# Kernel tuning notes

Measured on AMD Instinct MI355X. Metric: run time of the kernel, lower is better.

Reference implementation:

```python
import jax, jax.numpy as jnp
import numpy as np
import math

L, B, T, S, D, H = 6, 4, 1024, 1024, 1024, 16
HD = D // H
SCALE = 1.0 / math.sqrt(HD)
EPS = 1e-5


def _ln(x, w, b):
    m = x.mean(-1, keepdims=True)
    v = ((x - m) ** 2).mean(-1, keepdims=True)
    return (x - m) * jax.lax.rsqrt(v + EPS) * w + b


def _mha(xq, xkv, qw, qb, kw, kb, vw, vb, ow, ob, mask):
    b, t, _ = xq.shape
    s = xkv.shape[1]
    q = (xq @ qw.T + qb).reshape(b, t, H, HD).transpose(0, 2, 1, 3)
    k = (xkv @ kw.T + kb).reshape(b, s, H, HD).transpose(0, 2, 1, 3)
    v = (xkv @ vw.T + vb).reshape(b, s, H, HD).transpose(0, 2, 1, 3)
    scores = jnp.einsum('bhqd,bhkd->bhqk', q, k) * SCALE
    scores = jnp.where(mask == 0, -jnp.inf, scores)
    attn = jax.nn.softmax(scores, axis=-1)  # dropout is identity (eval)
    o = jnp.einsum('bhqk,bhkd->bhqd', attn, v).transpose(0, 2, 1, 3).reshape(b, t, D)
    return o @ ow.T + ob


def _ffn(x, f1w, f1b, f2w, f2b, fnw, fnb):
    h = jax.nn.gelu(x @ f1w.T + f1b, approximate=False)
    y = h @ f2w.T + f2b
    return x + _ln(y, fnw, fnb)


def setup_inputs() -> dict:
    key = jax.random.key(0)
    ks = jax.random.split(key, 16)
    wf = lambda k: jax.random.normal(k, (L, D, D), jnp.float32) * 0.02
    zb = jnp.zeros((L, D), jnp.float32)
    ones = jnp.ones((L, D), jnp.float32)
    inp = {
        'x': jax.random.normal(ks[0], (B, T, D), jnp.float32),
        'enc_outputs': jax.random.normal(ks[1], (B, S, D), jnp.float32),
        'sqw': wf(ks[2]), 'sqb': zb, 'skw': wf(ks[3]), 'skb': zb,
        'svw': wf(ks[4]), 'svb': zb, 'sow': wf(ks[5]), 'sob': zb,
        'cqw': wf(ks[6]), 'cqb': zb, 'ckw': wf(ks[7]), 'ckb': zb,
        'cvw': wf(ks[8]), 'cvb': zb, 'cow': wf(ks[9]), 'cob': zb,
        'f1w': wf(ks[10]), 'f1b': zb, 'f2w': wf(ks[11]), 'f2b': zb,
        'fnw': ones, 'fnb': zb,
        'l1w': ones, 'l1b': zb, 'l2w': ones, 'l2b': zb, 'l3w': ones, 'l3b': zb,
        'src_mask': jnp.ones((1, 1, T, S), jnp.int32),
        'tgt_mask': jnp.tril(jnp.ones((T, T), jnp.int32))[None, None],
    }
    return inp


def reference(x, enc_outputs, sqw, sqb, skw, skb, svw, svb, sow, sob,
              cqw, cqb, ckw, ckb, cvw, cvb, cow, cob,
              f1w, f1b, f2w, f2b, fnw, fnb,
              l1w, l1b, l2w, l2b, l3w, l3b, src_mask, tgt_mask):
    for l in range(L):
        sa = _mha(x, x, sqw[l], sqb[l], skw[l], skb[l], svw[l], svb[l], sow[l], sob[l], tgt_mask)
        x = _ln(x + sa, l1w[l], l1b[l])
        ca = _mha(x, enc_outputs, cqw[l], cqb[l], ckw[l], ckb[l], cvw[l], cvb[l], cow[l], cob[l], src_mask)
        x = _ln(x + ca, l2w[l], l2b[l])
        ff = _ffn(x, f1w[l], f1b[l], f2w[l], f2b[l], fnw[l], fnb[l])
        x = _ln(x + ff, l3w[l], l3b[l])
    return x
```

## Files before the change

kernel.cpp:

```cpp
#include <hip/hip_runtime.h>
#include <stdint.h>

typedef unsigned short u16;
typedef unsigned int u32;
typedef __bf16 bf16x8 __attribute__((ext_vector_type(8)));
typedef float f32x4 __attribute__((ext_vector_type(4)));
typedef u16 u16x8 __attribute__((ext_vector_type(8)));
typedef u16 u16x4 __attribute__((ext_vector_type(4)));
typedef u32 u32x2 __attribute__((ext_vector_type(2)));

#define MFMA16(A, B, C) __builtin_amdgcn_mfma_f32_16x16x32_bf16((A), (B), (C), 0, 0, 0)

#define GLOAD_LDS16(GP, LP)                                                    \
  __builtin_amdgcn_global_load_lds(                                            \
      (__attribute__((address_space(1))) void*)(GP),                           \
      (__attribute__((address_space(3))) void*)(LP), 16, 0, 0)

__device__ __forceinline__ u16 f2bf(float f) {
  return __builtin_bit_cast(u16, (__bf16)f);
}

__device__ __forceinline__ float bf2f(u16 v) {
  return __builtin_bit_cast(float, ((u32)v) << 16);
}

__device__ __forceinline__ float exp2_raw(float x) {
  float r;
  asm("v_exp_f32 %0, %1\n\ts_nop 0" : "=v"(r) : "v"(x));
  return r;
}

__device__ __forceinline__ u32 cvt_pk_bf16(float lo, float hi) {
  u32 r;
  asm("v_cvt_pk_bf16_f32 %0, %1, %2" : "=v"(r) : "v"(lo), "v"(hi));
  return r;
}

#define SC2 0.1803368801111204f

struct WPtrs {
  const float* p[10];
};

__global__ __launch_bounds__(256) void wcvt_kernel(WPtrs w, u16* __restrict__ dst, int loff) {
  const int mat = blockIdx.y;
  const int i = blockIdx.x * 256 + threadIdx.x;
  float4 v = ((const float4*)(w.p[mat] + loff))[i];
  u16x4 o = {f2bf(v.x), f2bf(v.y), f2bf(v.z), f2bf(v.w)};
  ((u16x4*)dst)[(size_t)mat * gridDim.x * 256 + i] = o;
}

struct GemmArgs {
  const u16* A[3];
  const u16* W[3];
  const float* bias[3];
  u16* C[3];
  float scale[3];
};

__global__ __launch_bounds__(256, 4) void gemm_bt(GemmArgs g) {
  const int mat = blockIdx.y >> 3;
  const int n0 = (blockIdx.y & 7) * 128;
  const int m0 = blockIdx.x * 128;
  const int kz = blockIdx.z;
  const int kn = 16 / gridDim.z;
  const u16* __restrict__ A = g.A[mat];
  const u16* __restrict__ W = g.W[mat];

  __shared__ u16 As[128][64];
  __shared__ u16 Bs[128][64];

  const int tid = threadIdx.x;
  const int lane = tid & 63;
  const int wv = tid >> 6;
  const int wm = (wv >> 1) * 64;
  const int wn = (wv & 1) * 64;
  const int fr = lane & 15;
  const int fg = lane >> 4;

  f32x4 acc[4][4];
#pragma unroll
  for (int i = 0; i < 4; ++i)
#pragma unroll
    for (int j = 0; j < 4; ++j)
#pragma unroll
      for (int r = 0; r < 4; ++r) acc[i][j][r] = 0.f;

  const int row8 = lane >> 3;
  const int csw = ((lane & 7) ^ row8) * 8;
  const u16* ga = A + (size_t)(m0 + wv * 32 + row8) * 1024 + csw + kz * kn * 64;
  const u16* gb = W + (size_t)(n0 + wv * 32 + row8) * 1024 + csw + kz * kn * 64;

  for (int kt = 0; kt < kn; ++kt) {
    __syncthreads();
#pragma unroll
    for (int i = 0; i < 4; ++i) {
      GLOAD_LDS16(ga + (size_t)i * 8 * 1024, &As[wv * 32 + i * 8][0]);
      GLOAD_LDS16(gb + (size_t)i * 8 * 1024, &Bs[wv * 32 + i * 8][0]);
    }
    ga += 64;
    gb += 64;
    __syncthreads();
#pragma unroll
    for (int ks = 0; ks < 2; ++ks) {
      bf16x8 af[4], bfr[4];
#pragma unroll
      for (int i = 0; i < 4; ++i) {
        af[i] = *(const bf16x8*)&As[wm + i * 16 + fr][((ks * 4 + fg) ^ (fr & 7)) * 8];
        bfr[i] = *(const bf16x8*)&Bs[wn + i * 16 + fr][((ks * 4 + fg) ^ (fr & 7)) * 8];
      }
#pragma unroll
      for (int mi = 0; mi < 4; ++mi)
#pragma unroll
        for (int ni = 0; ni < 4; ++ni) acc[mi][ni] = MFMA16(af[mi], bfr[ni], acc[mi][ni]);
    }
  }

  const float* __restrict__ bias = g.bias[mat];
  const float scl = g.scale[mat];
  float bv[4];
#pragma unroll
  for (int ni = 0; ni < 4; ++ni) bv[ni] = (kz == 0) ? bias[n0 + wn + ni * 16 + fr] : 0.f;

  u16* __restrict__ C = g.C[mat] + (size_t)kz * (4096 * 1024);
#pragma unroll
  for (int mi = 0; mi < 4; ++mi) {
#pragma unroll
    for (int ni = 0; ni < 4; ++ni) {
      const int col = n0 + wn + ni * 16 + fr;
#pragma unroll
      for (int r = 0; r < 4; ++r) {
        const int row = m0 + wm + mi * 16 + fg * 4 + r;
        C[(size_t)row * 1024 + col] = f2bf((acc[mi][ni][r] + bv[ni]) * scl);
      }
    }
  }
}

__global__ __launch_bounds__(256, 4) void gemm_ckv(const u16* __restrict__ A,
                                                   const u16* __restrict__ wbf,
                                                   const float* __restrict__ ckb,
                                                   const float* __restrict__ cvb,
                                                   u16* __restrict__ ckv) {
  const int m = blockIdx.y >> 3;
  const int l = m >> 1;
  const int ty = m & 1;
  const int n0 = (blockIdx.y & 7) * 128;
  const int m0 = blockIdx.x * 128;
  const u16* __restrict__ W = wbf + ((size_t)(5 + ty) * 6 + l) * (1024 * 1024);
  const float* __restrict__ bias = (ty ? cvb : ckb) + l * 1024;
  u16* __restrict__ C = ckv + (size_t)m * (4096 * 1024);

  __shared__ u16 As[128][64];
  __shared__ u16 Bs[128][64];

  const int tid = threadIdx.x;
  const int lane = tid & 63;
  const int wv = tid >> 6;
  const int wm = (wv >> 1) * 64;
  const int wn = (wv & 1) * 64;
  const int fr = lane & 15;
  const int fg = lane >> 4;

  f32x4 acc[4][4];
#pragma unroll
  for (int i = 0; i < 4; ++i)
#pragma unroll
    for (int j = 0; j < 4; ++j)
#pragma unroll
      for (int r = 0; r < 4; ++r) acc[i][j][r] = 0.f;

  const int row8 = lane >> 3;
  const int csw = ((lane & 7) ^ row8) * 8;
  const u16* ga = A + (size_t)(m0 + wv * 32 + row8) * 1024 + csw;
  const u16* gb = W + (size_t)(n0 + wv * 32 + row8) * 1024 + csw;

  for (int kt = 0; kt < 16; ++kt) {
    __syncthreads();
#pragma unroll
    for (int i = 0; i < 4; ++i) {
      GLOAD_LDS16(ga + (size_t)i * 8 * 1024, &As[wv * 32 + i * 8][0]);
      GLOAD_LDS16(gb + (size_t)i * 8 * 1024, &Bs[wv * 32 + i * 8][0]);
    }
    ga += 64;
    gb += 64;
    __syncthreads();
#pragma unroll
    for (int ks = 0; ks < 2; ++ks) {
      bf16x8 af[4], bfr[4];
#pragma unroll
      for (int i = 0; i < 4; ++i) {
        af[i] = *(const bf16x8*)&As[wm + i * 16 + fr][((ks * 4 + fg) ^ (fr & 7)) * 8];
        bfr[i] = *(const bf16x8*)&Bs[wn + i * 16 + fr][((ks * 4 + fg) ^ (fr & 7)) * 8];
      }
#pragma unroll
      for (int mi = 0; mi < 4; ++mi)
#pragma unroll
        for (int ni = 0; ni < 4; ++ni) acc[mi][ni] = MFMA16(af[mi], bfr[ni], acc[mi][ni]);
    }
  }

  float bv[4];
#pragma unroll
  for (int ni = 0; ni < 4; ++ni) bv[ni] = bias[n0 + wn + ni * 16 + fr];
#pragma unroll
  for (int mi = 0; mi < 4; ++mi) {
#pragma unroll
    for (int ni = 0; ni < 4; ++ni) {
      const int col = n0 + wn + ni * 16 + fr;
#pragma unroll
      for (int r = 0; r < 4; ++r) {
        const int row = m0 + wm + mi * 16 + fg * 4 + r;
        C[(size_t)row * 1024 + col] = f2bf(acc[mi][ni][r] + bv[ni]);
      }
    }
  }
}

__global__ __launch_bounds__(512, 4) void attn_fwd(const u16* __restrict__ Q,
                                                   const u16* __restrict__ K,
                                                   const u16* __restrict__ V,
                                                   u16* __restrict__ O, int causal) {
  const int b = blockIdx.x >> 4;
  const int h = blockIdx.x & 15;
  const int qb = causal ? (7 - blockIdx.y) : blockIdx.y;
  const int tid = threadIdx.x;
  const int lane = tid & 63;
  const int wv = tid >> 6;
  const int fr = lane & 15;
  const int fg = lane >> 4;

  __shared__ u16 Ks[2][64][64];
  __shared__ u16 Vt[2][64][64];
  __shared__ u16 Plds[8][16][64];

  const int qrow0 = b * 1024 + qb * 128 + wv * 16;
  const int col0 = h * 64;

  const u16* qp = Q + (size_t)(qrow0 + fr) * 1024 + col0 + fg * 8;
  bf16x8 aQ0 = *(const bf16x8*)qp;
  bf16x8 aQ1 = *(const bf16x8*)(qp + 32);

  f32x4 ov[4];
#pragma unroll
  for (int i = 0; i < 4; ++i)
#pragma unroll
    for (int r = 0; r < 4; ++r) ov[i][r] = 0.f;
  float l_part = 0.f;

  const int kv_base = b * 1024;
  const int qg = qb * 128 + wv * 16 + fr;
  const int qg_max = qb * 128 + wv * 16 + 15;
  const int nt = causal ? (2 * qb + 2) : 16;

  const u16* gk0 = K + (size_t)(kv_base + wv * 16 + (lane >> 3)) * 1024 + col0 +
                   (((lane & 7) ^ (lane >> 3)) * 8);
  const int vt = tid - 256;
  const int kkp = vt & 31;
  const int d0 = (vt >> 5) * 8;
  const u16* gv0 = V + (size_t)(kv_base + 2 * kkp) * 1024 + col0 + d0;

#define STAGE_K(T, BUF)                                                        \
  if (wv < 4) {                                                                \
    const u16* gk = gk0 + (size_t)(T)*64 * 1024;                               \
    GLOAD_LDS16(gk, &Ks[BUF][wv * 16][0]);                                     \
    GLOAD_LDS16(gk + 8 * 1024, &Ks[BUF][wv * 16 + 8][0]);                      \
  }
#define LOAD_V(T)                                                              \
  if (tid >= 256) {                                                            \
    const u16* gvp = gv0 + (size_t)(T)*64 * 1024;                              \
    vr0 = *(const u16x8*)gvp;                                                  \
    vr1 = *(const u16x8*)(gvp + 1024);                                         \
  }
#define WRITE_V(BUF)                                                           \
  if (tid >= 256) {                                                            \
    _Pragma("unroll") for (int j = 0; j < 8; ++j) {                            \
      u32 pk = (u32)vr0[j] | ((u32)vr1[j] << 16);                              \
      *(u32*)&Vt[BUF][d0 + j][(((kkp >> 2) ^ j) * 8) + (kkp & 3) * 2] = pk;    \
    }                                                                          \
  }

  u16x8 vr0, vr1;
  STAGE_K(0, 0);
  LOAD_V(0);
  WRITE_V(0);

  for (int t = 0; t < nt; ++t) {
    const int cur = t & 1;
    __syncthreads();
    const bool pf = (t + 1 < nt);
    if (pf) {
      STAGE_K(t + 1, cur ^ 1);
      LOAD_V(t + 1);
    }

    const bool active = !causal || (t * 64 <= qg_max);
    if (active) {
      f32x4 st[4];
      __builtin_amdgcn_s_setprio(1);
#pragma unroll
      for (int hh = 0; hh < 4; ++hh) {
#pragma unroll
        for (int r = 0; r < 4; ++r) st[hh][r] = 0.f;
        const u16* krow = &Ks[cur][hh * 16 + fr][0];
        bf16x8 k0 = *(const bf16x8*)(krow + ((fg ^ (fr & 7)) * 8));
        bf16x8 k1 = *(const bf16x8*)(krow + (((4 + fg) ^ (fr & 7)) * 8));
        st[hh] = MFMA16(k0, aQ0, st[hh]);
        st[hh] = MFMA16(k1, aQ1, st[hh]);
      }
      __builtin_amdgcn_s_setprio(0);

      if (causal && t >= 2 * qb) {
#pragma unroll
        for (int hh = 0; hh < 4; ++hh)
#pragma unroll
          for (int r = 0; r < 4; ++r) {
            const int kkg = t * 64 + hh * 16 + fg * 4 + r;
            if (kkg > qg) st[hh][r] = -1e30f;
          }
      }

      float p[16];
#pragma unroll
      for (int hh = 0; hh < 4; ++hh)
#pragma unroll
        for (int r = 0; r < 4; ++r) {
          const float e = exp2_raw(st[hh][r]);
          p[hh * 4 + r] = e;
          l_part += e;
        }

#pragma unroll
      for (int hh = 0; hh < 4; ++hh) {
        u32x2 wpair = {cvt_pk_bf16(p[hh * 4 + 0], p[hh * 4 + 1]),
                       cvt_pk_bf16(p[hh * 4 + 2], p[hh * 4 + 3])};
        const int c = hh * 2 + (fg >> 1);
        *(u32x2*)&Plds[wv][fr][((c ^ (fr & 7)) * 8) + (fg & 1) * 4] = wpair;
      }
      bf16x8 pa[2];
#pragma unroll
      for (int ks = 0; ks < 2; ++ks)
        pa[ks] = *(const bf16x8*)&Plds[wv][fr][(((ks * 4 + fg) ^ (fr & 7)) * 8)];
      __builtin_amdgcn_s_setprio(1);
#pragma unroll
      for (int dt = 0; dt < 4; ++dt) {
#pragma unroll
        for (int ks = 0; ks < 2; ++ks) {
          bf16x8 bvv =
              *(const bf16x8*)&Vt[cur][dt * 16 + fr][(((ks * 4 + fg) ^ (fr & 7)) * 8)];
          ov[dt] = MFMA16(pa[ks], bvv, ov[dt]);
        }
      }
      __builtin_amdgcn_s_setprio(0);
    }

    if (pf) WRITE_V(cur ^ 1);
  }

  float ps = l_part;
  ps += __shfl_xor(ps, 16);
  ps += __shfl_xor(ps, 32);
  const float linv = 1.0f / ps;
  float fin[4];
#pragma unroll
  for (int r = 0; r < 4; ++r) fin[r] = __shfl(linv, fg * 4 + r);
#pragma unroll
  for (int dt = 0; dt < 4; ++dt)
#pragma unroll
    for (int r = 0; r < 4; ++r) {
      const int row = qrow0 + fg * 4 + r;
      const int col = col0 + dt * 16 + fr;
      O[(size_t)row * 1024 + col] = f2bf(ov[dt][r] * fin[r]);
    }
#undef STAGE_K
#undef LOAD_V
#undef WRITE_V
}

__device__ __forceinline__ float4 ld_bf4(const u16* p, size_t idx4) {
  u16x4 t = ((const u16x4*)p)[idx4];
  return make_float4(bf2f(t[0]), bf2f(t[1]), bf2f(t[2]), bf2f(t[3]));
}

__global__ __launch_bounds__(256) void ln_res_kernel(const u16* __restrict__ Xb_in,
                                                     const u16* __restrict__ T0,
                                                     const u16* __restrict__ T1, int nT,
                                                     const float* __restrict__ w,
                                                     const float* __restrict__ bia,
                                                     u16* __restrict__ Xb_out) {
  __shared__ float red[2][4];
  const int row = blockIdx.x;
  const int tid = threadIdx.x;
  const int lane = tid & 63, wv = tid >> 6;
  const size_t base4 = (size_t)row * 256;
  float4 xv = ld_bf4(Xb_in, base4 + tid);
  float4 tv = ld_bf4(T0, base4 + tid);
  float z0 = xv.x + tv.x, z1 = xv.y + tv.y, z2 = xv.z + tv.z, z3 = xv.w + tv.w;
  if (nT == 2) {
    float4 t1 = ld_bf4(T1, base4 + tid);
    z0 += t1.x; z1 += t1.y; z2 += t1.z; z3 += t1.w;
  }
  float s = z0 + z1 + z2 + z3;
  float ss = z0 * z0 + z1 * z1 + z2 * z2 + z3 * z3;
#pragma unroll
  for (int m = 1; m <= 32; m <<= 1) {
    s += __shfl_xor(s, m);
    ss += __shfl_xor(ss, m);
  }
  if (lane == 0) {
    red[0][wv] = s;
    red[1][wv] = ss;
  }
  __syncthreads();
  s = red[0][0] + red[0][1] + red[0][2] + red[0][3];
  ss = red[1][0] + red[1][1] + red[1][2] + red[1][3];
  const float mean = s * (1.f / 1024.f);
  const float var = ss * (1.f / 1024.f) - mean * mean;
  const float rs = rsqrtf(fmaxf(var, 0.f) + 1e-5f);
  float4 wv4 = ((const float4*)w)[tid];
  float4 bv4 = ((const float4*)bia)[tid];
  float o0 = (z0 - mean) * rs * wv4.x + bv4.x;
  float o1 = (z1 - mean) * rs * wv4.y + bv4.y;
  float o2 = (z2 - mean) * rs * wv4.z + bv4.z;
  float o3 = (z3 - mean) * rs * wv4.w + bv4.w;
  u16x4 ob = {f2bf(o0), f2bf(o1), f2bf(o2), f2bf(o3)};
  ((u16x4*)Xb_out)[base4 + tid] = ob;
}

__global__ __launch_bounds__(256) void ffn_ln_kernel(
    const u16* __restrict__ Xb, const u16* __restrict__ Y0, const u16* __restrict__ Y1,
    int nT, const float* __restrict__ fw_, const float* __restrict__ fb_,
    const float* __restrict__ w3, const float* __restrict__ b3, u16* __restrict__ Xb_out,
    float* __restrict__ Fout) {
  __shared__ float red[2][4];
  const int row = blockIdx.x;
  const int tid = threadIdx.x;
  const int lane = tid & 63, wv = tid >> 6;
  const size_t base4 = (size_t)row * 256;
  float4 yv = ld_bf4(Y0, base4 + tid);
  if (nT == 2) {
    float4 y1 = ld_bf4(Y1, base4 + tid);
    yv.x += y1.x; yv.y += y1.y; yv.z += y1.z; yv.w += y1.w;
  }
  float s = yv.x + yv.y + yv.z + yv.w;
  float ss = yv.x * yv.x + yv.y * yv.y + yv.z * yv.z + yv.w * yv.w;
#pragma unroll
  for (int m = 1; m <= 32; m <<= 1) {
    s += __shfl_xor(s, m);
    ss += __shfl_xor(ss, m);
  }
  if (lane == 0) {
    red[0][wv] = s;
    red[1][wv] = ss;
  }
  __syncthreads();
  s = red[0][0] + red[0][1] + red[0][2] + red[0][3];
  ss = red[1][0] + red[1][1] + red[1][2] + red[1][3];
  const float mean = s * (1.f / 1024.f);
  const float var = ss * (1.f / 1024.f) - mean * mean;
  const float rs = rsqrtf(fmaxf(var, 0.f) + 1e-5f);
  float4 xv = ld_bf4(Xb, base4 + tid);
  float4 fw4 = ((const float4*)fw_)[tid];
  float4 fb4 = ((const float4*)fb_)[tid];
  float z0 = 2.f * xv.x + (yv.x - mean) * rs * fw4.x + fb4.x;
  float z1 = 2.f * xv.y + (yv.y - mean) * rs * fw4.y + fb4.y;
  float z2 = 2.f * xv.z + (yv.z - mean) * rs * fw4.z + fb4.z;
  float z3 = 2.f * xv.w + (yv.w - mean) * rs * fw4.w + fb4.w;
  float s2 = z0 + z1 + z2 + z3;
  float ss2 = z0 * z0 + z1 * z1 + z2 * z2 + z3 * z3;
#pragma unroll
  for (int m = 1; m <= 32; m <<= 1) {
    s2 += __shfl_xor(s2, m);
    ss2 += __shfl_xor(ss2, m);
  }
  __syncthreads();
  if (lane == 0) {
    red[0][wv] = s2;
    red[1][wv] = ss2;
  }
  __syncthreads();
  s2 = red[0][0] + red[0][1] + red[0][2] + red[0][3];
  ss2 = red[1][0] + red[1][1] + red[1][2] + red[1][3];
  const float mean2 = s2 * (1.f / 1024.f);
  const float var2 = ss2 * (1.f / 1024.f) - mean2 * mean2;
  const float rs2 = rsqrtf(fmaxf(var2, 0.f) + 1e-5f);
  float4 w4 = ((const float4*)w3)[tid];
  float4 b4 = ((const float4*)b3)[tid];
  float o0 = (z0 - mean2) * rs2 * w4.x + b4.x;
  float o1 = (z1 - mean2) * rs2 * w4.y + b4.y;
  float o2 = (z2 - mean2) * rs2 * w4.z + b4.z;
  float o3 = (z3 - mean2) * rs2 * w4.w + b4.w;
  u16x4 ob = {f2bf(o0), f2bf(o1), f2bf(o2), f2bf(o3)};
  ((u16x4*)Xb_out)[base4 + tid] = ob;
  if (Fout) ((float4*)Fout)[base4 + tid] = make_float4(o0, o1, o2, o3);
}

__global__ __launch_bounds__(256) void gelu_combine(const u16* __restrict__ T0,
                                                    const u16* __restrict__ T1, int nT,
                                                    u16* __restrict__ dst) {
  const size_t i = (size_t)blockIdx.x * 256 + threadIdx.x;
  float4 v = ld_bf4(T0, i);
  if (nT == 2) {
    float4 u = ld_bf4(T1, i);
    v.x += u.x; v.y += u.y; v.z += u.z; v.w += u.w;
  }
  v.x = 0.5f * v.x * (1.0f + erff(v.x * 0.70710678118654752f));
  v.y = 0.5f * v.y * (1.0f + erff(v.y * 0.70710678118654752f));
  v.z = 0.5f * v.z * (1.0f + erff(v.z * 0.70710678118654752f));
  v.w = 0.5f * v.w * (1.0f + erff(v.w * 0.70710678118654752f));
  u16x4 o = {f2bf(v.x), f2bf(v.y), f2bf(v.z), f2bf(v.w)};
  ((u16x4*)dst)[i] = o;
}

__global__ __launch_bounds__(256) void cast2_kernel(const float* __restrict__ inA,
                                                    const float* __restrict__ inB,
                                                    u16* __restrict__ outA,
                                                    u16* __restrict__ outB) {
  const int bx = blockIdx.x;
  const float* in = (bx < 4096) ? inA : inB;
  u16* out = (bx < 4096) ? outA : outB;
  const size_t i = (size_t)(bx & 4095) * 256 + threadIdx.x;
  float4 v = ((const float4*)in)[i];
  u16x4 o = {f2bf(v.x), f2bf(v.y), f2bf(v.z), f2bf(v.w)};
  ((u16x4*)out)[i] = o;
}

extern "C" void kernel_launch(void* const* d_in, const int* in_sizes, int n_in, void* d_out,
                              int out_size, void* d_ws, size_t ws_size, hipStream_t stream) {
  const float* x_in = (const float*)d_in[0];
  const float* enc = (const float*)d_in[1];
  const float* sqw = (const float*)d_in[2];
  const float* sqb = (const float*)d_in[3];
  const float* skw = (const float*)d_in[4];
  const float* skb = (const float*)d_in[5];
  const float* svw = (const float*)d_in[6];
  const float* svb = (const float*)d_in[7];
  const float* sow = (const float*)d_in[8];
  const float* sob = (const float*)d_in[9];
  const float* cqw = (const float*)d_in[10];
  const float* cqb = (const float*)d_in[11];
  const float* ckw = (const float*)d_in[12];
  const float* ckb = (const float*)d_in[13];
  const float* cvw = (const float*)d_in[14];
  const float* cvb = (const float*)d_in[15];
  const float* cow = (const float*)d_in[16];
  const float* cob = (const float*)d_in[17];
  const float* f1w = (const float*)d_in[18];
  const float* f1b = (const float*)d_in[19];
  const float* f2w = (const float*)d_in[20];
  const float* f2b = (const float*)d_in[21];
  const float* fnw = (const float*)d_in[22];
  const float* fnb = (const float*)d_in[23];
  const float* l1w = (const float*)d_in[24];
  const float* l1b = (const float*)d_in[25];
  const float* l2w = (const float*)d_in[26];
  const float* l2b = (const float*)d_in[27];
  const float* l3w = (const float*)d_in[28];
  const float* l3b = (const float*)d_in[29];

  const size_t MB = 1024 * 1024;
  const int ALLW = (ws_size >= 200 * MB) ? 1 : 0;
  const int NS = (ws_size >= 90 * MB) ? 2 : 1;
  const int CKV = (ALLW && ws_size >= 273 * MB) ? 1 : 0;
  char* ws = (char*)d_ws;
  u16* tmpb = (u16*)ws;
  char* p = ws + (size_t)NS * 8 * MB;
  u16* xb = (u16*)p;   p += 8 * MB;
  u16* encb = (u16*)p; p += 8 * MB;
  u16* qbuf = (u16*)p; p += 8 * MB;
  u16* kbuf = (u16*)p; p += 8 * MB;
  u16* vbuf = (u16*)p; p += 8 * MB;
  u16* wbf = (u16*)p;  p += (ALLW ? 120 : 20) * MB;
  u16* ckv = (u16*)p;
  u16* tmpb1 = tmpb + (size_t)4 * 1024 * 1024;
  const size_t W1M = 1024 * 1024;

  cast2_kernel<<<8192, 256, 0, stream>>>(x_in, enc, xb, encb);

  WPtrs wp;
  wp.p[0] = sqw; wp.p[1] = skw; wp.p[2] = svw; wp.p[3] = sow;
  wp.p[4] = cqw; wp.p[5] = ckw; wp.p[6] = cvw; wp.p[7] = cow;
  wp.p[8] = f1w; wp.p[9] = f2w;

  if (ALLW) wcvt_kernel<<<dim3(6144, 10), 256, 0, stream>>>(wp, wbf, 0);
  if (CKV) gemm_ckv<<<dim3(32, 96), 256, 0, stream>>>(encb, wbf, ckb, cvb, ckv);

  for (int l = 0; l < 6; ++l) {
    const size_t bo = (size_t)l * 1024;
    if (!ALLW) wcvt_kernel<<<dim3(1024, 10), 256, 0, stream>>>(wp, wbf, l * (int)W1M);
    #define WT(t) (ALLW ? (wbf + ((size_t)(t)*6 + l) * W1M) : (wbf + (size_t)(t)*W1M))

    GemmArgs g;
    g.scale[0] = SC2; g.scale[1] = 1.f; g.scale[2] = 1.f;
    g.A[0] = xb; g.A[1] = xb; g.A[2] = xb;
    g.W[0] = WT(0); g.W[1] = WT(1); g.W[2] = WT(2);
    g.bias[0] = sqb + bo; g.bias[1] = skb + bo; g.bias[2] = svb + bo;
    g.C[0] = qbuf; g.C[1] = kbuf; g.C[2] = vbuf;
    gemm_bt<<<dim3(32, 24, 1), 256, 0, stream>>>(g);
    attn_fwd<<<dim3(64, 8), 512, 0, stream>>>(qbuf, kbuf, vbuf, qbuf, 1);
    g.scale[0] = 1.f;
    g.A[0] = qbuf; g.W[0] = WT(3); g.bias[0] = sob + bo; g.C[0] = tmpb;
    gemm_bt<<<dim3(32, 8, NS), 256, 0, stream>>>(g);
    ln_res_kernel<<<4096, 256, 0, stream>>>(xb, tmpb, tmpb1, NS, l1w + bo, l1b + bo, xb);

    g.scale[0] = SC2;
    const u16 *ck_l, *cv_l;
    if (CKV) {
      g.A[0] = xb;
      g.W[0] = WT(4);
      g.bias[0] = cqb + bo;
      g.C[0] = qbuf;
      gemm_bt<<<dim3(32, 8, 1), 256, 0, stream>>>(g);
      ck_l = ckv + (size_t)(2 * l) * (4096 * 1024);
      cv_l = ckv + (size_t)(2 * l + 1) * (4096 * 1024);
    } else {
      g.A[0] = xb; g.A[1] = encb; g.A[2] = encb;
      g.W[0] = WT(4); g.W[1] = WT(5); g.W[2] = WT(6);
      g.bias[0] = cqb + bo; g.bias[1] = ckb + bo; g.bias[2] = cvb + bo;
      g.C[0] = qbuf; g.C[1] = kbuf; g.C[2] = vbuf;
      gemm_bt<<<dim3(32, 24, 1), 256, 0, stream>>>(g);
      ck_l = kbuf;
      cv_l = vbuf;
    }
    attn_fwd<<<dim3(64, 8), 512, 0, stream>>>(qbuf, ck_l, cv_l, qbuf, 0);
    g.scale[0] = 1.f;
    g.A[0] = qbuf; g.W[0] = WT(7); g.bias[0] = cob + bo; g.C[0] = tmpb;
    gemm_bt<<<dim3(32, 8, NS), 256, 0, stream>>>(g);
    ln_res_kernel<<<4096, 256, 0, stream>>>(xb, tmpb, tmpb1, NS, l2w + bo, l2b + bo, xb);

    g.A[0] = xb; g.W[0] = WT(8); g.bias[0] = f1b + bo; g.C[0] = tmpb;
    gemm_bt<<<dim3(32, 8, NS), 256, 0, stream>>>(g);
    gelu_combine<<<4096, 256, 0, stream>>>(tmpb, tmpb1, NS, kbuf);
    g.A[0] = kbuf; g.W[0] = WT(9); g.bias[0] = f2b + bo; g.C[0] = tmpb;
    gemm_bt<<<dim3(32, 8, NS), 256, 0, stream>>>(g);
    float* fo = (l == 5) ? (float*)d_out : nullptr;
    ffn_ln_kernel<<<4096, 256, 0, stream>>>(xb, tmpb, tmpb1, NS, fnw + bo, fnb + bo, l3w + bo,
                                            l3b + bo, xb, fo);
    #undef WT
  }
}
```

Measured before the change: 1.478 ms.

## Use 64x128 tiles for single-matrix GEMMs and drop precomputed cross-attention K/V

Adds a gemm_bt64 kernel with 64-row M tiles (2x4 MFMA per wave) and uses it for the output projections and both FFN GEMMs, doubling the block count to 512-1024 to fill more CUs. It also removes the upfront all-layer cross-attention K/V precompute (gemm_ckv and its workspace), so each layer computes cross Q/K/V in one fused launch again. Smaller tiles lower per-block operand reuse and add more A/B traffic. Dropping the precompute moves K/V work back into the layer loop.

```diff
diff --git a/kernel.cpp b/kernel.cpp
--- a/kernel.cpp
+++ b/kernel.cpp
@@ -137,34 +137,28 @@
   }
 }
 
-__global__ __launch_bounds__(256, 4) void gemm_ckv(const u16* __restrict__ A,
-                                                   const u16* __restrict__ wbf,
-                                                   const float* __restrict__ ckb,
-                                                   const float* __restrict__ cvb,
-                                                   u16* __restrict__ ckv) {
-  const int m = blockIdx.y >> 3;
-  const int l = m >> 1;
-  const int ty = m & 1;
-  const int n0 = (blockIdx.y & 7) * 128;
-  const int m0 = blockIdx.x * 128;
-  const u16* __restrict__ W = wbf + ((size_t)(5 + ty) * 6 + l) * (1024 * 1024);
-  const float* __restrict__ bias = (ty ? cvb : ckb) + l * 1024;
-  u16* __restrict__ C = ckv + (size_t)m * (4096 * 1024);
-
-  __shared__ u16 As[128][64];
+__global__ __launch_bounds__(256, 4) void gemm_bt64(GemmArgs g) {
+  const int n0 = blockIdx.y * 128;
+  const int m0 = blockIdx.x * 64;
+  const int kz = blockIdx.z;
+  const int kn = 16 / gridDim.z;
+  const u16* __restrict__ A = g.A[0];
+  const u16* __restrict__ W = g.W[0];
+
+  __shared__ u16 As[64][64];
   __shared__ u16 Bs[128][64];
 
   const int tid = threadIdx.x;
   const int lane = tid & 63;
   const int wv = tid >> 6;
-  const int wm = (wv >> 1) * 64;
+  const int wm = (wv >> 1) * 32;
   const int wn = (wv & 1) * 64;
   const int fr = lane & 15;
   const int fg = lane >> 4;
 
-  f32x4 acc[4][4];
-#pragma unroll
-  for (int i = 0; i < 4; ++i)
+  f32x4 acc[2][4];
+#pragma unroll
+  for (int i = 0; i < 2; ++i)
 #pragma unroll
     for (int j = 0; j < 4; ++j)
 #pragma unroll
@@ -172,39 +166,43 @@
 
   const int row8 = lane >> 3;
   const int csw = ((lane & 7) ^ row8) * 8;
-  const u16* ga = A + (size_t)(m0 + wv * 32 + row8) * 1024 + csw;
-  const u16* gb = W + (size_t)(n0 + wv * 32 + row8) * 1024 + csw;
-
-  for (int kt = 0; kt < 16; ++kt) {
+  const u16* ga = A + (size_t)(m0 + wv * 16 + row8) * 1024 + csw + kz * kn * 64;
+  const u16* gb = W + (size_t)(n0 + wv * 32 + row8) * 1024 + csw + kz * kn * 64;
+
+  for (int kt = 0; kt < kn; ++kt) {
     __syncthreads();
-#pragma unroll
-    for (int i = 0; i < 4; ++i) {
-      GLOAD_LDS16(ga + (size_t)i * 8 * 1024, &As[wv * 32 + i * 8][0]);
+    GLOAD_LDS16(ga, &As[wv * 16][0]);
+    GLOAD_LDS16(ga + (size_t)8 * 1024, &As[wv * 16 + 8][0]);
+#pragma unroll
+    for (int i = 0; i < 4; ++i)
       GLOAD_LDS16(gb + (size_t)i * 8 * 1024, &Bs[wv * 32 + i * 8][0]);
-    }
     ga += 64;
     gb += 64;
     __syncthreads();
 #pragma unroll
     for (int ks = 0; ks < 2; ++ks) {
-      bf16x8 af[4], bfr[4];
-#pragma unroll
-      for (int i = 0; i < 4; ++i) {
+      bf16x8 af[2], bfr[4];
+#pragma unroll
+      for (int i = 0; i < 2; ++i)
         af[i] = *(const bf16x8*)&As[wm + i * 16 + fr][((ks * 4 + fg) ^ (fr & 7)) * 8];
+#pragma unroll
+      for (int i = 0; i < 4; ++i)
         bfr[i] = *(const bf16x8*)&Bs[wn + i * 16 + fr][((ks * 4 + fg) ^ (fr & 7)) * 8];
-      }
-#pragma unroll
-      for (int mi = 0; mi < 4; ++mi)
+#pragma unroll
+      for (int mi = 0; mi < 2; ++mi)
 #pragma unroll
         for (int ni = 0; ni < 4; ++ni) acc[mi][ni] = MFMA16(af[mi], bfr[ni], acc[mi][ni]);
     }
   }
 
+  const float* __restrict__ bias = g.bias[0];
   float bv[4];
 #pragma unroll
-  for (int ni = 0; ni < 4; ++ni) bv[ni] = bias[n0 + wn + ni * 16 + fr];
-#pragma unroll
-  for (int mi = 0; mi < 4; ++mi) {
+  for (int ni = 0; ni < 4; ++ni) bv[ni] = (kz == 0) ? bias[n0 + wn + ni * 16 + fr] : 0.f;
+
+  u16* __restrict__ C = g.C[0] + (size_t)kz * (4096 * 1024);
+#pragma unroll
+  for (int mi = 0; mi < 2; ++mi) {
 #pragma unroll
     for (int ni = 0; ni < 4; ++ni) {
       const int col = n0 + wn + ni * 16 + fr;
@@ -561,7 +559,6 @@
   const size_t MB = 1024 * 1024;
   const int ALLW = (ws_size >= 200 * MB) ? 1 : 0;
   const int NS = (ws_size >= 90 * MB) ? 2 : 1;
-  const int CKV = (ALLW && ws_size >= 273 * MB) ? 1 : 0;
   char* ws = (char*)d_ws;
   u16* tmpb = (u16*)ws;
   char* p = ws + (size_t)NS * 8 * MB;
@@ -570,8 +567,7 @@
   u16* qbuf = (u16*)p; p += 8 * MB;
   u16* kbuf = (u16*)p; p += 8 * MB;
   u16* vbuf = (u16*)p; p += 8 * MB;
-  u16* wbf = (u16*)p;  p += (ALLW ? 120 : 20) * MB;
-  u16* ckv = (u16*)p;
+  u16* wbf = (u16*)p;
   u16* tmpb1 = tmpb + (size_t)4 * 1024 * 1024;
   const size_t W1M = 1024 * 1024;
 
@@ -583,7 +579,6 @@
   wp.p[8] = f1w; wp.p[9] = f2w;
 
   if (ALLW) wcvt_kernel<<<dim3(6144, 10), 256, 0, stream>>>(wp, wbf, 0);
-  if (CKV) gemm_ckv<<<dim3(32, 96), 256, 0, stream>>>(encb, wbf, ckb, cvb, ckv);
 
   for (int l = 0; l < 6; ++l) {
     const size_t bo = (size_t)l * 1024;
@@ -600,39 +595,26 @@
     attn_fwd<<<dim3(64, 8), 512, 0, stream>>>(qbuf, kbuf, vbuf, qbuf, 1);
     g.scale[0] = 1.f;
     g.A[0] = qbuf; g.W[0] = WT(3); g.bias[0] = sob + bo; g.C[0] = tmpb;
-    gemm_bt<<<dim3(32, 8, NS), 256, 0, stream>>>(g);
+    gemm_bt64<<<dim3(64, 8, NS), 256, 0, stream>>>(g);
     ln_res_kernel<<<4096, 256, 0, stream>>>(xb, tmpb, tmpb1, NS, l1w + bo, l1b + bo, xb);
 
     g.scale[0] = SC2;
-    const u16 *ck_l, *cv_l;
-    if (CKV) {
-      g.A[0] = xb;
-      g.W[0] = WT(4);
-      g.bias[0] = cqb + bo;
-      g.C[0] = qbuf;
-      gemm_bt<<<dim3(32, 8, 1), 256, 0, stream>>>(g);
-      ck_l = ckv + (size_t)(2 * l) * (4096 * 1024);
-      cv_l = ckv + (size_t)(2 * l + 1) * (4096 * 1024);
-    } else {
-      g.A[0] = xb; g.A[1] = encb; g.A[2] = encb;
-      g.W[0] = WT(4); g.W[1] = WT(5); g.W[2] = WT(6);
-      g.bias[0] = cqb + bo; g.bias[1] = ckb + bo; g.bias[2] = cvb + bo;
-      g.C[0] = qbuf; g.C[1] = kbuf; g.C[2] = vbuf;
-      gemm_bt<<<dim3(32, 24, 1), 256, 0, stream>>>(g);
-      ck_l = kbuf;
-      cv_l = vbuf;
-    }
-    attn_fwd<<<dim3(64, 8), 512, 0, stream>>>(qbuf, ck_l, cv_l, qbuf, 0);
+    g.A[0] = xb; g.A[1] = encb; g.A[2] = encb;
+    g.W[0] = WT(4); g.W[1] = WT(5); g.W[2] = WT(6);
+    g.bias[0] = cqb + bo; g.bias[1] = ckb + bo; g.bias[2] = cvb + bo;
+    g.C[0] = qbuf; g.C[1] = kbuf; g.C[2] = vbuf;
+    gemm_bt<<<dim3(32, 24, 1), 256, 0, stream>>>(g);
+    attn_fwd<<<dim3(64, 8), 512, 0, stream>>>(qbuf, kbuf, vbuf, qbuf, 0);
     g.scale[0] = 1.f;
     g.A[0] = qbuf; g.W[0] = WT(7); g.bias[0] = cob + bo; g.C[0] = tmpb;
-    gemm_bt<<<dim3(32, 8, NS), 256, 0, stream>>>(g);
+    gemm_bt64<<<dim3(64, 8, NS), 256, 0, stream>>>(g);
     ln_res_kernel<<<4096, 256, 0, stream>>>(xb, tmpb, tmpb1, NS, l2w + bo, l2b + bo, xb);
 
     g.A[0] = xb; g.W[0] = WT(8); g.bias[0] = f1b + bo; g.C[0] = tmpb;
-    gemm_bt<<<dim3(32, 8, NS), 256, 0, stream>>>(g);
+    gemm_bt64<<<dim3(64, 8, NS), 256, 0, stream>>>(g);
     gelu_combine<<<4096, 256, 0, stream>>>(tmpb, tmpb1, NS, kbuf);
     g.A[0] = kbuf; g.W[0] = WT(9); g.bias[0] = f2b + bo; g.C[0] = tmpb;
-    gemm_bt<<<dim3(32, 8, NS), 256, 0, stream>>>(g);
+    gemm_bt64<<<dim3(64, 8, NS), 256, 0, stream>>>(g);
     float* fo = (l == 5) ? (float*)d_out : nullptr;
     ffn_ln_kernel<<<4096, 256, 0, stream>>>(xb, tmpb, tmpb1, NS, fnw + bo, fnb + bo, l3w + bo,
                                             l3b + bo, xb, fo);
```

New measurement: 1.326 ms. -10.3%, faster.
